# Kernel tuning notes

Measured on AMD Instinct MI355X. Metric: run time of the kernel, lower is better.

The kernel has to match this reference:

```python
import jax, jax.numpy as jnp
import numpy as np

DIM = 384
HEADS = 12
W = 7  # window_size
N = W * W
B = 4096

def _relative_position_index(ws):
    ch = np.arange(ws)
    coords = np.stack(np.meshgrid(ch, ch, indexing='ij'))  # [2, W, W]
    cf = coords.reshape(2, -1)  # [2, W*W]
    rel = cf[:, :, None] - cf[:, None, :]  # [2, N, N]
    rel = rel.transpose(1, 2, 0)
    rel[:, :, 0] += ws - 1
    rel[:, :, 1] += ws - 1
    rel[:, :, 0] *= 2 * ws - 1
    return rel.sum(-1).astype(np.int32)  # [N, N]

def setup_inputs() -> dict:
    key = jax.random.key(0)
    ks = jax.random.split(key, 8)
    s = 0.02
    return {
        'x': jax.random.normal(ks[0], (B, N, DIM), jnp.float32),
        'y': jax.random.normal(ks[1], (B, N, DIM), jnp.float32),
        'q_w': jax.random.normal(ks[2], (DIM, DIM), jnp.float32) * s,
        'q_b': jnp.zeros((DIM,), jnp.float32),
        'kv_w': jax.random.normal(ks[3], (2 * DIM, DIM), jnp.float32) * s,
        'kv_b': jnp.zeros((2 * DIM,), jnp.float32),
        'proj_w': jax.random.normal(ks[4], (DIM, DIM), jnp.float32) * s,
        'proj_b': jnp.zeros((DIM,), jnp.float32),
        'rel_table': jax.random.normal(ks[5], ((2 * W - 1) ** 2, HEADS), jnp.float32) * s,
        'rel_index': jnp.asarray(_relative_position_index(W)),
    }

def reference(x, y, q_w, q_b, kv_w, kv_b, proj_w, proj_b, rel_table, rel_index):
    Bx, N1, C = x.shape
    N2 = y.shape[1]
    hd = C // HEADS
    scale = hd ** -0.5
    # projections (torch Linear: x @ W^T + b)
    q = (x @ q_w.T + q_b).reshape(Bx, N1, HEADS, hd)
    kv = (y @ kv_w.T + kv_b).reshape(Bx, N2, 2, HEADS, hd)
    k = kv[:, :, 0]  # [B, N2, H, d]
    v = kv[:, :, 1]
    attn = jnp.einsum('bqhd,bkhd->bhqk', q, k) * scale
    # relative position bias: [N1, N2, H] -> [H, N1, N2]
    bias = rel_table[rel_index.reshape(-1)].reshape(N1, N2, HEADS)
    attn = attn + jnp.transpose(bias, (2, 0, 1))[None]
    attn = jax.nn.softmax(attn, axis=-1)
    out = jnp.einsum('bhqk,bkhd->bqhd', attn, v).reshape(Bx, N1, C)
    return out @ proj_w.T + proj_b
```

## Files before the change

kernel.cpp:

```cpp
#include <hip/hip_runtime.h>

#define DIM 384
#define HEADS 12
#define HD 32
#define NTOK 49
#define NWIN 4096
#define MTOT (NWIN*NTOK)
#define PSTR 72

typedef __attribute__((ext_vector_type(8))) __bf16 bf16x8;
typedef __attribute__((ext_vector_type(4))) __bf16 bf16x4;
typedef __attribute__((ext_vector_type(4))) float f32x4;

static __device__ __forceinline__ f32x4 mfma16(bf16x8 a, bf16x8 b, f32x4 c) {
  return __builtin_amdgcn_mfma_f32_16x16x32_bf16(a, b, c, 0, 0, 0);
}

static __device__ __forceinline__ void gload_lds16(const void* g, void* l) {
  __builtin_amdgcn_global_load_lds(
      (const __attribute__((address_space(1))) unsigned int*)g,
      (__attribute__((address_space(3))) unsigned int*)l, 16, 0, 0);
}

static __device__ __forceinline__ bf16x4 cvt4(float4 v) {
  bf16x4 t;
  t[0]=(__bf16)v.x; t[1]=(__bf16)v.y; t[2]=(__bf16)v.z; t[3]=(__bf16)v.w;
  return t;
}

__global__ void k_prep(const float* __restrict__ qw, const float* __restrict__ kvw,
                       const float* __restrict__ pw, const float* __restrict__ rel_table,
                       const int* __restrict__ rel_index,
                       __bf16* __restrict__ qw_bf, __bf16* __restrict__ kvw_bf,
                       __bf16* __restrict__ pw_bf, float* __restrict__ bias_pad) {
  int i = blockIdx.x * 256 + threadIdx.x;
  if (i < DIM*DIM)   qw_bf[i] = (__bf16)qw[i];
  if (i < 2*DIM*DIM) kvw_bf[i] = (__bf16)kvw[i];
  if (i < DIM*DIM)   pw_bf[i] = (__bf16)pw[i];
  if (i < HEADS*64*64) {
    int h = i >> 12, rem = i & 4095, q = rem >> 6, k = rem & 63;
    float v;
    if (k >= NTOK)      v = -1e30f;
    else if (q >= NTOK) v = 0.0f;
    else v = rel_table[rel_index[q*NTOK + k] * HEADS + h];
    bias_pad[i] = v;
  }
}

__global__ __launch_bounds__(256, 4) void k_qkv(
    const float* __restrict__ x, const float* __restrict__ y,
    const __bf16* __restrict__ qw_bf, const __bf16* __restrict__ kvw_bf,
    const float* __restrict__ q_b, const float* __restrict__ kv_b,
    __bf16* __restrict__ Qws, __bf16* __restrict__ Kws, __bf16* __restrict__ Vws)
{
  int b = blockIdx.x;
  int orig = (b & 7) * 1764 + (b >> 3);
  int mtile = orig / 9;
  int nt9 = orig - mtile*9;
  const float* A; const __bf16* Bw; const float* bias; __bf16* Cout;
  int wrow0, col0;
  if (nt9 < 3) { A = x; Bw = qw_bf; bias = q_b; Cout = Qws; wrow0 = nt9*128; col0 = wrow0; }
  else {
    A = y; Bw = kvw_bf; bias = kv_b; wrow0 = (nt9-3)*128;
    if (wrow0 < DIM) { Cout = Kws; col0 = wrow0; } else { Cout = Vws; col0 = wrow0 - DIM; }
  }
  bias += wrow0;

  __shared__ __align__(16) __bf16 As[2*128*32];
  __shared__ __align__(16) __bf16 Bs[3*128*32];

  int t = threadIdx.x, lane = t & 63, wave = t >> 6;
  int l15 = lane & 15, g = lane >> 4;
  int wr = (wave >> 1) * 64, wc = (wave & 1) * 64;
  int row0b = mtile*128;

  int c8 = lane & 7;
  int r8 = lane >> 3;
  int swk = (lane >> 4) & 3;
  const float* asrc = A + (size_t)(row0b + wave*32 + r8)*DIM + c8*4;
  unsigned lwb = (unsigned)wave*2048 + (unsigned)r8*64
               + ((((c8 >> 1) ^ swk) << 4) + (c8 & 1)*8);

  int sr  = 2*(lane >> 3) + ((lane >> 2) & 1);
  int scb = (lane & 3) ^ ((lane >> 3) & 3);
  const __bf16* bsrc0 = Bw + (size_t)(wrow0 + (wave*2    )*16 + sr)*DIM + scb*8;
  const __bf16* bsrc1 = Bw + (size_t)(wrow0 + (wave*2 + 1)*16 + sr)*DIM + scb*8;

  f32x4 acc[4][4];
  #pragma unroll
  for (int a=0;a<4;a++)
    #pragma unroll
    for (int bb=0;bb<4;bb++) acc[a][bb] = (f32x4){0.f,0.f,0.f,0.f};

  {
    float4 s0 = *(const float4*)(asrc);
    float4 s1 = *(const float4*)(asrc +  8*DIM);
    float4 s2 = *(const float4*)(asrc + 16*DIM);
    float4 s3 = *(const float4*)(asrc + 24*DIM);
    gload_lds16(bsrc0,      (char*)Bs +        (wave*2  )*1024);
    gload_lds16(bsrc1,      (char*)Bs +        (wave*2+1)*1024);
    gload_lds16(bsrc0 + 32, (char*)Bs + 8192 + (wave*2  )*1024);
    gload_lds16(bsrc1 + 32, (char*)Bs + 8192 + (wave*2+1)*1024);
    *(bf16x4*)((char*)As + lwb +    0) = cvt4(s0);
    *(bf16x4*)((char*)As + lwb +  512) = cvt4(s1);
    *(bf16x4*)((char*)As + lwb + 1024) = cvt4(s2);
    *(bf16x4*)((char*)As + lwb + 1536) = cvt4(s3);
    asm volatile("s_waitcnt vmcnt(2)" ::: "memory");
    asm volatile("s_waitcnt lgkmcnt(0)" ::: "memory");
    __builtin_amdgcn_s_barrier();
  }

  int lslot = l15*64 + ((g ^ ((l15 >> 1) & 3)) << 4);

  #pragma unroll
  for (int kt = 0; kt < 12; ++kt) {
    const int cur2 = kt & 1, nxt2 = cur2 ^ 1;
    const int cur3 = kt % 3, pre3 = (kt + 2) % 3;
    float4 s0, s1, s2, s3;
    if (kt < 11) {
      int kk = (kt + 1) * 32;
      s0 = *(const float4*)(asrc + kk);
      s1 = *(const float4*)(asrc + kk +  8*DIM);
      s2 = *(const float4*)(asrc + kk + 16*DIM);
      s3 = *(const float4*)(asrc + kk + 24*DIM);
    }
    if (kt < 10) {
      int kk = (kt + 2) * 32;
      gload_lds16(bsrc0 + kk, (char*)Bs + pre3*8192 + (wave*2  )*1024);
      gload_lds16(bsrc1 + kk, (char*)Bs + pre3*8192 + (wave*2+1)*1024);
    }
    bf16x8 af[4], bfv[4];
    #pragma unroll
    for (int a=0;a<4;a++)
      af[a]  = *(const bf16x8*)((const char*)As + cur2*8192 + (wr + a*16)*64 + lslot);
    #pragma unroll
    for (int bb=0;bb<4;bb++)
      bfv[bb] = *(const bf16x8*)((const char*)Bs + cur3*8192 + (wc + bb*16)*64 + lslot);
    #pragma unroll
    for (int a=0;a<4;a++)
      #pragma unroll
      for (int bb=0;bb<4;bb++)
        acc[a][bb] = mfma16(af[a], bfv[bb], acc[a][bb]);
    if (kt < 11) {
      *(bf16x4*)((char*)As + nxt2*8192 + lwb +    0) = cvt4(s0);
      *(bf16x4*)((char*)As + nxt2*8192 + lwb +  512) = cvt4(s1);
      *(bf16x4*)((char*)As + nxt2*8192 + lwb + 1024) = cvt4(s2);
      *(bf16x4*)((char*)As + nxt2*8192 + lwb + 1536) = cvt4(s3);
      if (kt < 10) asm volatile("s_waitcnt vmcnt(2)" ::: "memory");
      else         asm volatile("s_waitcnt vmcnt(0)" ::: "memory");
      asm volatile("s_waitcnt lgkmcnt(0)" ::: "memory");
      __builtin_amdgcn_s_barrier();
    }
  }

  #pragma unroll
  for (int a=0;a<4;a++) {
    #pragma unroll
    for (int bb=0;bb<4;bb++) {
      int colw = wc + bb*16 + l15;
      float bi = bias[colw];
      size_t cbase = (size_t)(row0b + wr + a*16 + 4*g)*DIM + (col0 + colw);
      #pragma unroll
      for (int r=0;r<4;r++)
        Cout[cbase + (size_t)r*DIM] = (__bf16)(acc[a][bb][r] + bi);
    }
  }
}

__global__ __launch_bounds__(256) void k_attn(
    __bf16* qao,
    const __bf16* __restrict__ Kws, const __bf16* __restrict__ Vws,
    const float* __restrict__ bias_pad)
{
  __shared__ __align__(16) __bf16 Psh[4][64*PSTR];
  __shared__ __align__(16) __bf16 VTsh[4][32*PSTR];
  int b = blockIdx.x;
  int lane = threadIdx.x & 63, wave = threadIdx.x >> 6;
  int l15 = lane & 15, g = lane >> 4;
  __bf16* Pw  = Psh[wave];
  __bf16* VTw = VTsh[wave];
  size_t rowbase = (size_t)b * NTOK * DIM;
  const float scale = 0.17677669529663687f;

  for (int e = lane; e < 32*15; e += 64) {
    int d = e / 15, k = 49 + (e - d*15);
    VTw[d*PSTR + k] = (__bf16)0.0f;
  }

  for (int hh = 0; hh < 3; hh++) {
    int h = wave + hh*4;
    for (int e = lane; e < NTOK*HD; e += 64) {
      int k = e >> 5, d = e & 31;
      VTw[d*PSTR + k] = Vws[rowbase + (size_t)k*DIM + h*HD + d];
    }
    bf16x8 qf[4], kf[4];
    #pragma unroll
    for (int mt=0; mt<4; mt++) {
      int q = 16*mt + l15; if (q > 48) q = 48;
      qf[mt] = *(const bf16x8*)(qao + rowbase + (size_t)q*DIM + h*HD + g*8);
    }
    #pragma unroll
    for (int nt=0; nt<4; nt++) {
      int kk = 16*nt + l15; if (kk > 48) kk = 48;
      kf[nt] = *(const bf16x8*)(Kws + rowbase + (size_t)kk*DIM + h*HD + g*8);
    }
    f32x4 sacc[4][4];
    #pragma unroll
    for (int mt=0; mt<4; mt++)
      #pragma unroll
      for (int nt=0; nt<4; nt++)
        sacc[mt][nt] = mfma16(qf[mt], kf[nt], (f32x4){0.f,0.f,0.f,0.f});

    const float* bt = bias_pad + h*4096;
    float rs[4][4];
    #pragma unroll
    for (int mt=0; mt<4; mt++) {
      #pragma unroll
      for (int r=0; r<4; r++) {
        int q = 16*mt + 4*g + r;
        float v0 = sacc[mt][0][r]*scale + bt[q*64 +  0 + l15];
        float v1 = sacc[mt][1][r]*scale + bt[q*64 + 16 + l15];
        float v2 = sacc[mt][2][r]*scale + bt[q*64 + 32 + l15];
        float v3 = sacc[mt][3][r]*scale + bt[q*64 + 48 + l15];
        float m = fmaxf(fmaxf(v0,v1), fmaxf(v2,v3));
        #pragma unroll
        for (int off=1; off<16; off<<=1) m = fmaxf(m, __shfl_xor(m, off));
        v0 = __expf(v0-m); v1 = __expf(v1-m); v2 = __expf(v2-m); v3 = __expf(v3-m);
        float s = v0+v1+v2+v3;
        #pragma unroll
        for (int off=1; off<16; off<<=1) s += __shfl_xor(s, off);
        rs[mt][r] = s;
        Pw[q*PSTR +  0 + l15] = (__bf16)v0;
        Pw[q*PSTR + 16 + l15] = (__bf16)v1;
        Pw[q*PSTR + 32 + l15] = (__bf16)v2;
        Pw[q*PSTR + 48 + l15] = (__bf16)v3;
      }
    }

    #pragma unroll
    for (int mt=0; mt<4; mt++) {
      #pragma unroll
      for (int dt=0; dt<2; dt++) {
        f32x4 o = (f32x4){0.f,0.f,0.f,0.f};
        #pragma unroll
        for (int ks=0; ks<2; ks++) {
          bf16x8 pa = *(const bf16x8*)(Pw  + (16*mt + l15)*PSTR + 32*ks + 8*g);
          bf16x8 vb = *(const bf16x8*)(VTw + (16*dt + l15)*PSTR + 32*ks + 8*g);
          o = mfma16(pa, vb, o);
        }
        #pragma unroll
        for (int r=0; r<4; r++) {
          int q = 16*mt + 4*g + r;
          if (q < NTOK)
            qao[rowbase + (size_t)q*DIM + h*HD + 16*dt + l15] = (__bf16)(o[r] / rs[mt][r]);
        }
      }
    }
  }
}

__global__ __launch_bounds__(256, 4) void k_proj(
    const __bf16* __restrict__ Aao, const __bf16* __restrict__ pw_bf,
    const float* __restrict__ pb, float* __restrict__ out)
{
  int b = blockIdx.x;
  int orig = (b & 7) * 588 + (b >> 3);
  int mtile = orig / 3;
  int nt = orig - mtile*3;
  int lane = threadIdx.x & 63, wave = threadIdx.x >> 6;
  int l15 = lane & 15, g = lane >> 4;
  int wr = (wave >> 1) * 64, wc = (wave & 1) * 64;
  int row0b = mtile*128;
  int col00 = nt*128;

  __shared__ __align__(16) __bf16 As[3*128*32];
  __shared__ __align__(16) __bf16 Bs[3*128*32];

  int sr  = 2*(lane >> 3) + ((lane >> 2) & 1);
  int scb = (lane & 3) ^ ((lane >> 3) & 3);
  const __bf16* asrc0 = Aao   + (size_t)(row0b + (wave*2    )*16 + sr)*DIM + scb*8;
  const __bf16* asrc1 = Aao   + (size_t)(row0b + (wave*2 + 1)*16 + sr)*DIM + scb*8;
  const __bf16* bsrc0 = pw_bf + (size_t)(col00 + (wave*2    )*16 + sr)*DIM + scb*8;
  const __bf16* bsrc1 = pw_bf + (size_t)(col00 + (wave*2 + 1)*16 + sr)*DIM + scb*8;

  f32x4 acc[4][4];
  #pragma unroll
  for (int a=0;a<4;a++)
    #pragma unroll
    for (int bb=0;bb<4;bb++) acc[a][bb] = (f32x4){0.f,0.f,0.f,0.f};

  {
    gload_lds16(asrc0,      (char*)As +        (wave*2  )*1024);
    gload_lds16(asrc1,      (char*)As +        (wave*2+1)*1024);
    gload_lds16(bsrc0,      (char*)Bs +        (wave*2  )*1024);
    gload_lds16(bsrc1,      (char*)Bs +        (wave*2+1)*1024);
    gload_lds16(asrc0 + 32, (char*)As + 8192 + (wave*2  )*1024);
    gload_lds16(asrc1 + 32, (char*)As + 8192 + (wave*2+1)*1024);
    gload_lds16(bsrc0 + 32, (char*)Bs + 8192 + (wave*2  )*1024);
    gload_lds16(bsrc1 + 32, (char*)Bs + 8192 + (wave*2+1)*1024);
    asm volatile("s_waitcnt vmcnt(4)" ::: "memory");
    __builtin_amdgcn_s_barrier();
  }

  int lslot = l15*64 + ((g ^ ((l15 >> 1) & 3)) << 4);

  #pragma unroll
  for (int kt = 0; kt < 12; ++kt) {
    const int cur3 = kt % 3, pre3 = (kt + 2) % 3;
    if (kt < 10) {
      int kk = (kt + 2) * 32;
      gload_lds16(asrc0 + kk, (char*)As + pre3*8192 + (wave*2  )*1024);
      gload_lds16(asrc1 + kk, (char*)As + pre3*8192 + (wave*2+1)*1024);
      gload_lds16(bsrc0 + kk, (char*)Bs + pre3*8192 + (wave*2  )*1024);
      gload_lds16(bsrc1 + kk, (char*)Bs + pre3*8192 + (wave*2+1)*1024);
    }
    bf16x8 af[4], bfv[4];
    #pragma unroll
    for (int a=0;a<4;a++)
      af[a]  = *(const bf16x8*)((const char*)As + cur3*8192 + (wr + a*16)*64 + lslot);
    #pragma unroll
    for (int bb=0;bb<4;bb++)
      bfv[bb] = *(const bf16x8*)((const char*)Bs + cur3*8192 + (wc + bb*16)*64 + lslot);
    #pragma unroll
    for (int a=0;a<4;a++)
      #pragma unroll
      for (int bb=0;bb<4;bb++)
        acc[a][bb] = mfma16(af[a], bfv[bb], acc[a][bb]);
    if (kt < 11) {
      if (kt < 10) asm volatile("s_waitcnt vmcnt(4)" ::: "memory");
      else         asm volatile("s_waitcnt vmcnt(0)" ::: "memory");
      __builtin_amdgcn_s_barrier();
    }
  }

  #pragma unroll
  for (int a=0;a<4;a++) {
    #pragma unroll
    for (int bb=0;bb<4;bb++) {
      int col = col00 + wc + bb*16 + l15;
      float bi = pb[col];
      size_t cbase = (size_t)(row0b + wr + a*16 + 4*g)*DIM + col;
      #pragma unroll
      for (int r=0;r<4;r++)
        out[cbase + (size_t)r*DIM] = acc[a][bb][r] + bi;
    }
  }
}

extern "C" void kernel_launch(void* const* d_in, const int* in_sizes, int n_in,
                              void* d_out, int out_size, void* d_ws, size_t ws_size,
                              hipStream_t stream)
{
  const float* x   = (const float*)d_in[0];
  const float* y   = (const float*)d_in[1];
  const float* qw  = (const float*)d_in[2];
  const float* qb  = (const float*)d_in[3];
  const float* kvw = (const float*)d_in[4];
  const float* kvb = (const float*)d_in[5];
  const float* pw  = (const float*)d_in[6];
  const float* pb  = (const float*)d_in[7];
  const float* rt  = (const float*)d_in[8];
  const int*   ri  = (const int*)d_in[9];
  float* out = (float*)d_out;

  char* ws = (char*)d_ws;
  const size_t WS_NEEDED = 1376256ull + 3ull*154140672ull;
  if (ws_size < WS_NEEDED) return;

  __bf16* qw_bf    = (__bf16*)(ws);
  __bf16* kvw_bf   = (__bf16*)(ws + 294912);
  __bf16* pw_bf    = (__bf16*)(ws + 884736);
  float*  bias_pad = (float*)(ws + 1179648);
  __bf16* Qws      = (__bf16*)(ws + 1376256);
  __bf16* Kws      = Qws + (size_t)MTOT*DIM;
  __bf16* Vws      = Kws + (size_t)MTOT*DIM;

  k_prep<<<dim3(1152), dim3(256), 0, stream>>>(qw, kvw, pw, rt, ri, qw_bf, kvw_bf, pw_bf, bias_pad);
  k_qkv <<<dim3(1568*9), dim3(256), 0, stream>>>(x, y, qw_bf, kvw_bf, qb, kvb, Qws, Kws, Vws);
  k_attn<<<dim3(NWIN), dim3(256), 0, stream>>>(Qws, Kws, Vws, bias_pad);
  k_proj<<<dim3(1568*3), dim3(256), 0, stream>>>(Qws, pw_bf, pb, out);
}
```

Before: 840.8 us.

## Store Q/K/V and attention output in head-major per-window layout

The projection GEMM epilogue now writes Q, K and V as [window][head][token][dim], using a magic-number divide by 49 in place of row-major [token][384]. The attention kernel therefore reads each head's data as one contiguous block, with vectorized V loads for the transpose. The output projection reads its A operand from this layout, where each 32-wide K slice is a separate head block. The aim is better coalescing in the attention kernel, at the cost of scattered 2-byte stores in the GEMM epilogue and strided A tile loads in the projection.

```diff
diff --git a/kernel.cpp b/kernel.cpp
--- a/kernel.cpp
+++ b/kernel.cpp
@@ -7,6 +7,8 @@
 #define NWIN 4096
 #define MTOT (NWIN*NTOK)
 #define PSTR 72
+#define WSTR 18816
+#define HSTR 1568
 
 typedef __attribute__((ext_vector_type(8))) __bf16 bf16x8;
 typedef __attribute__((ext_vector_type(4))) __bf16 bf16x4;
@@ -26,6 +28,11 @@
   bf16x4 t;
   t[0]=(__bf16)v.x; t[1]=(__bf16)v.y; t[2]=(__bf16)v.z; t[3]=(__bf16)v.w;
   return t;
+}
+
+static __device__ __forceinline__ void div49(unsigned r, unsigned& w, unsigned& t) {
+  w = (unsigned)(((unsigned long long)r * 1402438302ull) >> 36);
+  t = r - w * 49u;
 }
 
 __global__ void k_prep(const float* __restrict__ qw, const float* __restrict__ kvw,
@@ -153,16 +160,26 @@
     }
   }
 
+  unsigned wo[4][4];
+  #pragma unroll
+  for (int a=0;a<4;a++)
+    #pragma unroll
+    for (int r=0;r<4;r++) {
+      unsigned row = (unsigned)(row0b + wr + a*16 + 4*g + r);
+      unsigned w, tk; div49(row, w, tk);
+      wo[a][r] = w*(unsigned)WSTR + tk*32u;
+    }
   #pragma unroll
   for (int a=0;a<4;a++) {
     #pragma unroll
     for (int bb=0;bb<4;bb++) {
       int colw = wc + bb*16 + l15;
+      int col = col0 + colw;
+      unsigned hb = (unsigned)(col >> 5)*(unsigned)HSTR + (unsigned)(col & 31);
       float bi = bias[colw];
-      size_t cbase = (size_t)(row0b + wr + a*16 + 4*g)*DIM + (col0 + colw);
       #pragma unroll
       for (int r=0;r<4;r++)
-        Cout[cbase + (size_t)r*DIM] = (__bf16)(acc[a][bb][r] + bi);
+        Cout[wo[a][r] + hb] = (__bf16)(acc[a][bb][r] + bi);
     }
   }
 }
@@ -179,7 +196,9 @@
   int l15 = lane & 15, g = lane >> 4;
   __bf16* Pw  = Psh[wave];
   __bf16* VTw = VTsh[wave];
-  size_t rowbase = (size_t)b * NTOK * DIM;
+  __bf16* Qb = qao + (size_t)b * WSTR;
+  const __bf16* Kb = Kws + (size_t)b * WSTR;
+  const __bf16* Vb = Vws + (size_t)b * WSTR;
   const float scale = 0.17677669529663687f;
 
   for (int e = lane; e < 32*15; e += 64) {
@@ -189,20 +208,25 @@
 
   for (int hh = 0; hh < 3; hh++) {
     int h = wave + hh*4;
-    for (int e = lane; e < NTOK*HD; e += 64) {
-      int k = e >> 5, d = e & 31;
-      VTw[d*PSTR + k] = Vws[rowbase + (size_t)k*DIM + h*HD + d];
+    const __bf16* Qh = Qb + h*HSTR;
+    const __bf16* Kh = Kb + h*HSTR;
+    const __bf16* Vh = Vb + h*HSTR;
+    for (int e = lane*8; e < NTOK*HD; e += 512) {
+      bf16x8 v = *(const bf16x8*)(Vh + e);
+      int tok = e >> 5, d0 = e & 31;
+      #pragma unroll
+      for (int i=0;i<8;i++) VTw[(d0+i)*PSTR + tok] = v[i];
     }
     bf16x8 qf[4], kf[4];
     #pragma unroll
     for (int mt=0; mt<4; mt++) {
       int q = 16*mt + l15; if (q > 48) q = 48;
-      qf[mt] = *(const bf16x8*)(qao + rowbase + (size_t)q*DIM + h*HD + g*8);
+      qf[mt] = *(const bf16x8*)(Qh + q*HD + g*8);
     }
     #pragma unroll
     for (int nt=0; nt<4; nt++) {
       int kk = 16*nt + l15; if (kk > 48) kk = 48;
-      kf[nt] = *(const bf16x8*)(Kws + rowbase + (size_t)kk*DIM + h*HD + g*8);
+      kf[nt] = *(const bf16x8*)(Kh + kk*HD + g*8);
     }
     f32x4 sacc[4][4];
     #pragma unroll
@@ -237,6 +261,7 @@
       }
     }
 
+    __bf16* AOh = Qb + h*HSTR;
     #pragma unroll
     for (int mt=0; mt<4; mt++) {
       #pragma unroll
@@ -252,7 +277,7 @@
         for (int r=0; r<4; r++) {
           int q = 16*mt + 4*g + r;
           if (q < NTOK)
-            qao[rowbase + (size_t)q*DIM + h*HD + 16*dt + l15] = (__bf16)(o[r] / rs[mt][r]);
+            AOh[q*HD + 16*dt + l15] = (__bf16)(o[r] / rs[mt][r]);
         }
       }
     }
@@ -278,8 +303,14 @@
 
   int sr  = 2*(lane >> 3) + ((lane >> 2) & 1);
   int scb = (lane & 3) ^ ((lane >> 3) & 3);
-  const __bf16* asrc0 = Aao   + (size_t)(row0b + (wave*2    )*16 + sr)*DIM + scb*8;
-  const __bf16* asrc1 = Aao   + (size_t)(row0b + (wave*2 + 1)*16 + sr)*DIM + scb*8;
+  const __bf16* asrc0; const __bf16* asrc1;
+  {
+    unsigned r0 = (unsigned)(row0b + (wave*2    )*16 + sr);
+    unsigned r1 = (unsigned)(row0b + (wave*2 + 1)*16 + sr);
+    unsigned w0, t0, w1, t1; div49(r0, w0, t0); div49(r1, w1, t1);
+    asrc0 = Aao + (size_t)w0*WSTR + t0*32 + scb*8;
+    asrc1 = Aao + (size_t)w1*WSTR + t1*32 + scb*8;
+  }
   const __bf16* bsrc0 = pw_bf + (size_t)(col00 + (wave*2    )*16 + sr)*DIM + scb*8;
   const __bf16* bsrc1 = pw_bf + (size_t)(col00 + (wave*2 + 1)*16 + sr)*DIM + scb*8;
 
@@ -290,14 +321,14 @@
     for (int bb=0;bb<4;bb++) acc[a][bb] = (f32x4){0.f,0.f,0.f,0.f};
 
   {
-    gload_lds16(asrc0,      (char*)As +        (wave*2  )*1024);
-    gload_lds16(asrc1,      (char*)As +        (wave*2+1)*1024);
-    gload_lds16(bsrc0,      (char*)Bs +        (wave*2  )*1024);
-    gload_lds16(bsrc1,      (char*)Bs +        (wave*2+1)*1024);
-    gload_lds16(asrc0 + 32, (char*)As + 8192 + (wave*2  )*1024);
-    gload_lds16(asrc1 + 32, (char*)As + 8192 + (wave*2+1)*1024);
-    gload_lds16(bsrc0 + 32, (char*)Bs + 8192 + (wave*2  )*1024);
-    gload_lds16(bsrc1 + 32, (char*)Bs + 8192 + (wave*2+1)*1024);
+    gload_lds16(asrc0,        (char*)As +        (wave*2  )*1024);
+    gload_lds16(asrc1,        (char*)As +        (wave*2+1)*1024);
+    gload_lds16(bsrc0,        (char*)Bs +        (wave*2  )*1024);
+    gload_lds16(bsrc1,        (char*)Bs +        (wave*2+1)*1024);
+    gload_lds16(asrc0 + HSTR, (char*)As + 8192 + (wave*2  )*1024);
+    gload_lds16(asrc1 + HSTR, (char*)As + 8192 + (wave*2+1)*1024);
+    gload_lds16(bsrc0 + 32,   (char*)Bs + 8192 + (wave*2  )*1024);
+    gload_lds16(bsrc1 + 32,   (char*)Bs + 8192 + (wave*2+1)*1024);
     asm volatile("s_waitcnt vmcnt(4)" ::: "memory");
     __builtin_amdgcn_s_barrier();
   }
@@ -308,11 +339,12 @@
   for (int kt = 0; kt < 12; ++kt) {
     const int cur3 = kt % 3, pre3 = (kt + 2) % 3;
     if (kt < 10) {
-      int kk = (kt + 2) * 32;
-      gload_lds16(asrc0 + kk, (char*)As + pre3*8192 + (wave*2  )*1024);
-      gload_lds16(asrc1 + kk, (char*)As + pre3*8192 + (wave*2+1)*1024);
-      gload_lds16(bsrc0 + kk, (char*)Bs + pre3*8192 + (wave*2  )*1024);
-      gload_lds16(bsrc1 + kk, (char*)Bs + pre3*8192 + (wave*2+1)*1024);
+      int ka = (kt + 2) * HSTR;
+      int kb = (kt + 2) * 32;
+      gload_lds16(asrc0 + ka, (char*)As + pre3*8192 + (wave*2  )*1024);
+      gload_lds16(asrc1 + ka, (char*)As + pre3*8192 + (wave*2+1)*1024);
+      gload_lds16(bsrc0 + kb, (char*)Bs + pre3*8192 + (wave*2  )*1024);
+      gload_lds16(bsrc1 + kb, (char*)Bs + pre3*8192 + (wave*2+1)*1024);
     }
     bf16x8 af[4], bfv[4];
     #pragma unroll
```

Measured after the change: 1.039 ms. 23.5% more time.

## Enlarge QKV GEMM tile to 256x128 with 512-thread blocks

Applied to the files above, without the earlier changes.

The QKV projection kernel now uses 8 waves per block covering a 256-row M tile instead of 128, with the A tile in LDS doubled and the load mapping and swizzle rewritten so each wave loads rows strided by 64. Each block's B (weight) tile is reused across twice as many rows, and global weight traffic per output is halved. The cost is more LDS per block and more registers under launch bounds of 512 threads with 4 blocks, which may cut occupancy, plus half as many blocks.

```diff
diff --git a/kernel.cpp b/kernel.cpp
--- a/kernel.cpp
+++ b/kernel.cpp
@@ -47,14 +47,14 @@
   }
 }
 
-__global__ __launch_bounds__(256, 4) void k_qkv(
+__global__ __launch_bounds__(512, 4) void k_qkv(
     const float* __restrict__ x, const float* __restrict__ y,
     const __bf16* __restrict__ qw_bf, const __bf16* __restrict__ kvw_bf,
     const float* __restrict__ q_b, const float* __restrict__ kv_b,
     __bf16* __restrict__ Qws, __bf16* __restrict__ Kws, __bf16* __restrict__ Vws)
 {
   int b = blockIdx.x;
-  int orig = (b & 7) * 1764 + (b >> 3);
+  int orig = (b & 7) * 882 + (b >> 3);
   int mtile = orig / 9;
   int nt9 = orig - mtile*9;
   const float* A; const __bf16* Bw; const float* bias; __bf16* Cout;
@@ -66,25 +66,25 @@
   }
   bias += wrow0;
 
-  __shared__ __align__(16) __bf16 As[2*128*32];
+  __shared__ __align__(16) __bf16 As[2*256*32];
   __shared__ __align__(16) __bf16 Bs[3*128*32];
 
   int t = threadIdx.x, lane = t & 63, wave = t >> 6;
   int l15 = lane & 15, g = lane >> 4;
-  int wr = (wave >> 1) * 64, wc = (wave & 1) * 64;
-  int row0b = mtile*128;
+  int wrM = (wave >> 1) * 64;
+  int wcN = (wave & 1) * 64;
+  int row0b = mtile*256;
 
   int c8 = lane & 7;
   int r8 = lane >> 3;
-  int swk = (lane >> 4) & 3;
-  const float* asrc = A + (size_t)(row0b + wave*32 + r8)*DIM + c8*4;
-  unsigned lwb = (unsigned)wave*2048 + (unsigned)r8*64
+  int swk = ((wave*8 + r8) >> 1) & 3;
+  const float* asrc = A + (size_t)(row0b + wave*8 + r8)*DIM + c8*4;
+  unsigned lwb = (unsigned)(wave*8 + r8)*64
                + ((((c8 >> 1) ^ swk) << 4) + (c8 & 1)*8);
 
   int sr  = 2*(lane >> 3) + ((lane >> 2) & 1);
   int scb = (lane & 3) ^ ((lane >> 3) & 3);
-  const __bf16* bsrc0 = Bw + (size_t)(wrow0 + (wave*2    )*16 + sr)*DIM + scb*8;
-  const __bf16* bsrc1 = Bw + (size_t)(wrow0 + (wave*2 + 1)*16 + sr)*DIM + scb*8;
+  const __bf16* bsrc = Bw + (size_t)(wrow0 + wave*16 + sr)*DIM + scb*8;
 
   f32x4 acc[4][4];
   #pragma unroll
@@ -94,18 +94,16 @@
 
   {
     float4 s0 = *(const float4*)(asrc);
-    float4 s1 = *(const float4*)(asrc +  8*DIM);
-    float4 s2 = *(const float4*)(asrc + 16*DIM);
-    float4 s3 = *(const float4*)(asrc + 24*DIM);
-    gload_lds16(bsrc0,      (char*)Bs +        (wave*2  )*1024);
-    gload_lds16(bsrc1,      (char*)Bs +        (wave*2+1)*1024);
-    gload_lds16(bsrc0 + 32, (char*)Bs + 8192 + (wave*2  )*1024);
-    gload_lds16(bsrc1 + 32, (char*)Bs + 8192 + (wave*2+1)*1024);
-    *(bf16x4*)((char*)As + lwb +    0) = cvt4(s0);
-    *(bf16x4*)((char*)As + lwb +  512) = cvt4(s1);
-    *(bf16x4*)((char*)As + lwb + 1024) = cvt4(s2);
-    *(bf16x4*)((char*)As + lwb + 1536) = cvt4(s3);
-    asm volatile("s_waitcnt vmcnt(2)" ::: "memory");
+    float4 s1 = *(const float4*)(asrc +  64*DIM);
+    float4 s2 = *(const float4*)(asrc + 128*DIM);
+    float4 s3 = *(const float4*)(asrc + 192*DIM);
+    gload_lds16(bsrc,      (char*)Bs +        wave*1024);
+    gload_lds16(bsrc + 32, (char*)Bs + 8192 + wave*1024);
+    *(bf16x4*)((char*)As + lwb +     0) = cvt4(s0);
+    *(bf16x4*)((char*)As + lwb +  4096) = cvt4(s1);
+    *(bf16x4*)((char*)As + lwb +  8192) = cvt4(s2);
+    *(bf16x4*)((char*)As + lwb + 12288) = cvt4(s3);
+    asm volatile("s_waitcnt vmcnt(1)" ::: "memory");
     asm volatile("s_waitcnt lgkmcnt(0)" ::: "memory");
     __builtin_amdgcn_s_barrier();
   }
@@ -120,33 +118,32 @@
     if (kt < 11) {
       int kk = (kt + 1) * 32;
       s0 = *(const float4*)(asrc + kk);
-      s1 = *(const float4*)(asrc + kk +  8*DIM);
-      s2 = *(const float4*)(asrc + kk + 16*DIM);
-      s3 = *(const float4*)(asrc + kk + 24*DIM);
-    }
-    if (kt < 10) {
-      int kk = (kt + 2) * 32;
-      gload_lds16(bsrc0 + kk, (char*)Bs + pre3*8192 + (wave*2  )*1024);
-      gload_lds16(bsrc1 + kk, (char*)Bs + pre3*8192 + (wave*2+1)*1024);
-    }
+      s1 = *(const float4*)(asrc + kk +  64*DIM);
+      s2 = *(const float4*)(asrc + kk + 128*DIM);
+      s3 = *(const float4*)(asrc + kk + 192*DIM);
+    }
+    if (kt < 10)
+      gload_lds16(bsrc + (kt + 2)*32, (char*)Bs + pre3*8192 + wave*1024);
+
     bf16x8 af[4], bfv[4];
     #pragma unroll
     for (int a=0;a<4;a++)
-      af[a]  = *(const bf16x8*)((const char*)As + cur2*8192 + (wr + a*16)*64 + lslot);
+      af[a]  = *(const bf16x8*)((const char*)As + cur2*16384 + (wrM + a*16)*64 + lslot);
     #pragma unroll
     for (int bb=0;bb<4;bb++)
-      bfv[bb] = *(const bf16x8*)((const char*)Bs + cur3*8192 + (wc + bb*16)*64 + lslot);
+      bfv[bb] = *(const bf16x8*)((const char*)Bs + cur3*8192 + (wcN + bb*16)*64 + lslot);
     #pragma unroll
     for (int a=0;a<4;a++)
       #pragma unroll
       for (int bb=0;bb<4;bb++)
         acc[a][bb] = mfma16(af[a], bfv[bb], acc[a][bb]);
+
     if (kt < 11) {
-      *(bf16x4*)((char*)As + nxt2*8192 + lwb +    0) = cvt4(s0);
-      *(bf16x4*)((char*)As + nxt2*8192 + lwb +  512) = cvt4(s1);
-      *(bf16x4*)((char*)As + nxt2*8192 + lwb + 1024) = cvt4(s2);
-      *(bf16x4*)((char*)As + nxt2*8192 + lwb + 1536) = cvt4(s3);
-      if (kt < 10) asm volatile("s_waitcnt vmcnt(2)" ::: "memory");
+      *(bf16x4*)((char*)As + nxt2*16384 + lwb +     0) = cvt4(s0);
+      *(bf16x4*)((char*)As + nxt2*16384 + lwb +  4096) = cvt4(s1);
+      *(bf16x4*)((char*)As + nxt2*16384 + lwb +  8192) = cvt4(s2);
+      *(bf16x4*)((char*)As + nxt2*16384 + lwb + 12288) = cvt4(s3);
+      if (kt < 10) asm volatile("s_waitcnt vmcnt(1)" ::: "memory");
       else         asm volatile("s_waitcnt vmcnt(0)" ::: "memory");
       asm volatile("s_waitcnt lgkmcnt(0)" ::: "memory");
       __builtin_amdgcn_s_barrier();
@@ -157,9 +154,9 @@
   for (int a=0;a<4;a++) {
     #pragma unroll
     for (int bb=0;bb<4;bb++) {
-      int colw = wc + bb*16 + l15;
+      int colw = wcN + bb*16 + l15;
       float bi = bias[colw];
-      size_t cbase = (size_t)(row0b + wr + a*16 + 4*g)*DIM + (col0 + colw);
+      size_t cbase = (size_t)(row0b + wrM + a*16 + 4*g)*DIM + (col0 + colw);
       #pragma unroll
       for (int r=0;r<4;r++)
         Cout[cbase + (size_t)r*DIM] = (__bf16)(acc[a][bb][r] + bi);
@@ -376,7 +373,7 @@
   __bf16* Vws      = Kws + (size_t)MTOT*DIM;
 
   k_prep<<<dim3(1152), dim3(256), 0, stream>>>(qw, kvw, pw, rt, ri, qw_bf, kvw_bf, pw_bf, bias_pad);
-  k_qkv <<<dim3(1568*9), dim3(256), 0, stream>>>(x, y, qw_bf, kvw_bf, qb, kvb, Qws, Kws, Vws);
+  k_qkv <<<dim3(784*9), dim3(512), 0, stream>>>(x, y, qw_bf, kvw_bf, qb, kvb, Qws, Kws, Vws);
   k_attn<<<dim3(NWIN), dim3(256), 0, stream>>>(Qws, Kws, Vws, bias_pad);
   k_proj<<<dim3(1568*3), dim3(256), 0, stream>>>(Qws, pw_bf, pb, out);
 }
```

Measured after the change: 851.6 us. Within noise of the previous version (+1.3%).

## Fuse attention and output projection into one per-window kernel

Applied to the files above, without the earlier changes.

Merges the attention kernel and the separate output-projection GEMM. Each window's attention output now stays in an LDS buffer (64 rows, padded stride) instead of being written to global memory and read back. After a block barrier, each wave computes 96 output columns for the window and streams proj weights straight from global/L2 with register double-buffering. The P scratch is cut to a 16-row tile per m-tile so the larger LDS footprint fits two blocks per CU. The risks are lower occupancy, proj weights re-read from cache by every window, and a less efficient 49-row GEMM tile compared with the tuned 128x128 LDS-pipelined GEMM.

```diff
diff --git a/kernel.cpp b/kernel.cpp
--- a/kernel.cpp
+++ b/kernel.cpp
@@ -7,6 +7,7 @@
 #define NWIN 4096
 #define MTOT (NWIN*NTOK)
 #define PSTR 72
+#define ASTR 392
 
 typedef __attribute__((ext_vector_type(8))) __bf16 bf16x8;
 typedef __attribute__((ext_vector_type(4))) __bf16 bf16x4;
@@ -167,13 +168,15 @@
   }
 }
 
-__global__ __launch_bounds__(256) void k_attn(
-    __bf16* qao,
-    const __bf16* __restrict__ Kws, const __bf16* __restrict__ Vws,
-    const float* __restrict__ bias_pad)
+__global__ __launch_bounds__(256, 2) void k_attnproj(
+    const __bf16* __restrict__ Qws, const __bf16* __restrict__ Kws,
+    const __bf16* __restrict__ Vws, const float* __restrict__ bias_pad,
+    const __bf16* __restrict__ pw_bf, const float* __restrict__ pb,
+    float* __restrict__ out)
 {
-  __shared__ __align__(16) __bf16 Psh[4][64*PSTR];
   __shared__ __align__(16) __bf16 VTsh[4][32*PSTR];
+  __shared__ __align__(16) __bf16 Psh[4][16*PSTR];
+  __shared__ __align__(16) __bf16 AOB[64*ASTR];
   int b = blockIdx.x;
   int lane = threadIdx.x & 63, wave = threadIdx.x >> 6;
   int l15 = lane & 15, g = lane >> 4;
@@ -197,7 +200,7 @@
     #pragma unroll
     for (int mt=0; mt<4; mt++) {
       int q = 16*mt + l15; if (q > 48) q = 48;
-      qf[mt] = *(const bf16x8*)(qao + rowbase + (size_t)q*DIM + h*HD + g*8);
+      qf[mt] = *(const bf16x8*)(Qws + rowbase + (size_t)q*DIM + h*HD + g*8);
     }
     #pragma unroll
     for (int nt=0; nt<4; nt++) {
@@ -212,12 +215,13 @@
         sacc[mt][nt] = mfma16(qf[mt], kf[nt], (f32x4){0.f,0.f,0.f,0.f});
 
     const float* bt = bias_pad + h*4096;
-    float rs[4][4];
     #pragma unroll
     for (int mt=0; mt<4; mt++) {
+      float rs[4];
       #pragma unroll
       for (int r=0; r<4; r++) {
         int q = 16*mt + 4*g + r;
+        int qloc = 4*g + r;
         float v0 = sacc[mt][0][r]*scale + bt[q*64 +  0 + l15];
         float v1 = sacc[mt][1][r]*scale + bt[q*64 + 16 + l15];
         float v2 = sacc[mt][2][r]*scale + bt[q*64 + 32 + l15];
@@ -229,120 +233,76 @@
         float s = v0+v1+v2+v3;
         #pragma unroll
         for (int off=1; off<16; off<<=1) s += __shfl_xor(s, off);
-        rs[mt][r] = s;
-        Pw[q*PSTR +  0 + l15] = (__bf16)v0;
-        Pw[q*PSTR + 16 + l15] = (__bf16)v1;
-        Pw[q*PSTR + 32 + l15] = (__bf16)v2;
-        Pw[q*PSTR + 48 + l15] = (__bf16)v3;
+        rs[r] = s;
+        Pw[qloc*PSTR +  0 + l15] = (__bf16)v0;
+        Pw[qloc*PSTR + 16 + l15] = (__bf16)v1;
+        Pw[qloc*PSTR + 32 + l15] = (__bf16)v2;
+        Pw[qloc*PSTR + 48 + l15] = (__bf16)v3;
       }
-    }
-
-    #pragma unroll
-    for (int mt=0; mt<4; mt++) {
       #pragma unroll
       for (int dt=0; dt<2; dt++) {
         f32x4 o = (f32x4){0.f,0.f,0.f,0.f};
         #pragma unroll
         for (int ks=0; ks<2; ks++) {
-          bf16x8 pa = *(const bf16x8*)(Pw  + (16*mt + l15)*PSTR + 32*ks + 8*g);
+          bf16x8 pa = *(const bf16x8*)(Pw  + l15*PSTR + 32*ks + 8*g);
           bf16x8 vb = *(const bf16x8*)(VTw + (16*dt + l15)*PSTR + 32*ks + 8*g);
           o = mfma16(pa, vb, o);
         }
         #pragma unroll
         for (int r=0; r<4; r++) {
-          int q = 16*mt + 4*g + r;
-          if (q < NTOK)
-            qao[rowbase + (size_t)q*DIM + h*HD + 16*dt + l15] = (__bf16)(o[r] / rs[mt][r]);
+          int tok = 16*mt + 4*g + r;
+          AOB[(unsigned)tok*ASTR + h*HD + 16*dt + l15] = (__bf16)(o[r] / rs[r]);
         }
       }
     }
   }
-}
-
-__global__ __launch_bounds__(256, 4) void k_proj(
-    const __bf16* __restrict__ Aao, const __bf16* __restrict__ pw_bf,
-    const float* __restrict__ pb, float* __restrict__ out)
-{
-  int b = blockIdx.x;
-  int orig = (b & 7) * 588 + (b >> 3);
-  int mtile = orig / 3;
-  int nt = orig - mtile*3;
-  int lane = threadIdx.x & 63, wave = threadIdx.x >> 6;
-  int l15 = lane & 15, g = lane >> 4;
-  int wr = (wave >> 1) * 64, wc = (wave & 1) * 64;
-  int row0b = mtile*128;
-  int col00 = nt*128;
-
-  __shared__ __align__(16) __bf16 As[3*128*32];
-  __shared__ __align__(16) __bf16 Bs[3*128*32];
-
-  int sr  = 2*(lane >> 3) + ((lane >> 2) & 1);
-  int scb = (lane & 3) ^ ((lane >> 3) & 3);
-  const __bf16* asrc0 = Aao   + (size_t)(row0b + (wave*2    )*16 + sr)*DIM + scb*8;
-  const __bf16* asrc1 = Aao   + (size_t)(row0b + (wave*2 + 1)*16 + sr)*DIM + scb*8;
-  const __bf16* bsrc0 = pw_bf + (size_t)(col00 + (wave*2    )*16 + sr)*DIM + scb*8;
-  const __bf16* bsrc1 = pw_bf + (size_t)(col00 + (wave*2 + 1)*16 + sr)*DIM + scb*8;
-
-  f32x4 acc[4][4];
-  #pragma unroll
-  for (int a=0;a<4;a++)
-    #pragma unroll
-    for (int bb=0;bb<4;bb++) acc[a][bb] = (f32x4){0.f,0.f,0.f,0.f};
+  __syncthreads();
 
   {
-    gload_lds16(asrc0,      (char*)As +        (wave*2  )*1024);
-    gload_lds16(asrc1,      (char*)As +        (wave*2+1)*1024);
-    gload_lds16(bsrc0,      (char*)Bs +        (wave*2  )*1024);
-    gload_lds16(bsrc1,      (char*)Bs +        (wave*2+1)*1024);
-    gload_lds16(asrc0 + 32, (char*)As + 8192 + (wave*2  )*1024);
-    gload_lds16(asrc1 + 32, (char*)As + 8192 + (wave*2+1)*1024);
-    gload_lds16(bsrc0 + 32, (char*)Bs + 8192 + (wave*2  )*1024);
-    gload_lds16(bsrc1 + 32, (char*)Bs + 8192 + (wave*2+1)*1024);
-    asm volatile("s_waitcnt vmcnt(4)" ::: "memory");
-    __builtin_amdgcn_s_barrier();
-  }
-
-  int lslot = l15*64 + ((g ^ ((l15 >> 1) & 3)) << 4);
-
-  #pragma unroll
-  for (int kt = 0; kt < 12; ++kt) {
-    const int cur3 = kt % 3, pre3 = (kt + 2) % 3;
-    if (kt < 10) {
-      int kk = (kt + 2) * 32;
-      gload_lds16(asrc0 + kk, (char*)As + pre3*8192 + (wave*2  )*1024);
-      gload_lds16(asrc1 + kk, (char*)As + pre3*8192 + (wave*2+1)*1024);
-      gload_lds16(bsrc0 + kk, (char*)Bs + pre3*8192 + (wave*2  )*1024);
-      gload_lds16(bsrc1 + kk, (char*)Bs + pre3*8192 + (wave*2+1)*1024);
-    }
-    bf16x8 af[4], bfv[4];
+    f32x4 acc[4][6];
     #pragma unroll
     for (int a=0;a<4;a++)
-      af[a]  = *(const bf16x8*)((const char*)As + cur3*8192 + (wr + a*16)*64 + lslot);
-    #pragma unroll
-    for (int bb=0;bb<4;bb++)
-      bfv[bb] = *(const bf16x8*)((const char*)Bs + cur3*8192 + (wc + bb*16)*64 + lslot);
-    #pragma unroll
-    for (int a=0;a<4;a++)
-      #pragma unroll
-      for (int bb=0;bb<4;bb++)
-        acc[a][bb] = mfma16(af[a], bfv[bb], acc[a][bb]);
-    if (kt < 11) {
-      if (kt < 10) asm volatile("s_waitcnt vmcnt(4)" ::: "memory");
-      else         asm volatile("s_waitcnt vmcnt(0)" ::: "memory");
-      __builtin_amdgcn_s_barrier();
-    }
-  }
-
-  #pragma unroll
-  for (int a=0;a<4;a++) {
-    #pragma unroll
-    for (int bb=0;bb<4;bb++) {
-      int col = col00 + wc + bb*16 + l15;
-      float bi = pb[col];
-      size_t cbase = (size_t)(row0b + wr + a*16 + 4*g)*DIM + col;
-      #pragma unroll
-      for (int r=0;r<4;r++)
-        out[cbase + (size_t)r*DIM] = acc[a][bb][r] + bi;
+      #pragma unroll
+      for (int j=0;j<6;j++) acc[a][j] = (f32x4){0.f,0.f,0.f,0.f};
+    const __bf16* bptr[6];
+    #pragma unroll
+    for (int j=0;j<6;j++)
+      bptr[j] = pw_bf + (size_t)(96*wave + 16*j + l15)*DIM + g*8;
+    bf16x8 bc[6];
+    #pragma unroll
+    for (int j=0;j<6;j++) bc[j] = *(const bf16x8*)(bptr[j]);
+
+    #pragma unroll
+    for (int kt = 0; kt < 12; ++kt) {
+      bf16x8 bn[6];
+      if (kt < 11) {
+        #pragma unroll
+        for (int j=0;j<6;j++) bn[j] = *(const bf16x8*)(bptr[j] + (kt+1)*32);
+      }
+      bf16x8 af[4];
+      #pragma unroll
+      for (int a=0;a<4;a++)
+        af[a] = *(const bf16x8*)(AOB + (unsigned)(16*a + l15)*ASTR + kt*32 + g*8);
+      #pragma unroll
+      for (int a=0;a<4;a++)
+        #pragma unroll
+        for (int j=0;j<6;j++)
+          acc[a][j] = mfma16(af[a], bc[j], acc[a][j]);
+      #pragma unroll
+      for (int j=0;j<6;j++) bc[j] = bn[j];
+    }
+    #pragma unroll
+    for (int j=0;j<6;j++) {
+      const int col = 96*wave + 16*j + l15;
+      const float bi = pb[col];
+      #pragma unroll
+      for (int a=0;a<4;a++)
+        #pragma unroll
+        for (int r=0;r<4;r++) {
+          const int tok = 16*a + 4*g + r;
+          if (tok < NTOK)
+            out[((size_t)b*NTOK + tok)*DIM + col] = acc[a][j][r] + bi;
+        }
     }
   }
 }
@@ -375,8 +335,7 @@
   __bf16* Kws      = Qws + (size_t)MTOT*DIM;
   __bf16* Vws      = Kws + (size_t)MTOT*DIM;
 
-  k_prep<<<dim3(1152), dim3(256), 0, stream>>>(qw, kvw, pw, rt, ri, qw_bf, kvw_bf, pw_bf, bias_pad);
-  k_qkv <<<dim3(1568*9), dim3(256), 0, stream>>>(x, y, qw_bf, kvw_bf, qb, kvb, Qws, Kws, Vws);
-  k_attn<<<dim3(NWIN), dim3(256), 0, stream>>>(Qws, Kws, Vws, bias_pad);
-  k_proj<<<dim3(1568*3), dim3(256), 0, stream>>>(Qws, pw_bf, pb, out);
-}
+  k_prep    <<<dim3(1152), dim3(256), 0, stream>>>(qw, kvw, pw, rt, ri, qw_bf, kvw_bf, pw_bf, bias_pad);
+  k_qkv     <<<dim3(1568*9), dim3(256), 0, stream>>>(x, y, qw_bf, kvw_bf, qb, kvb, Qws, Kws, Vws);
+  k_attnproj<<<dim3(NWIN), dim3(256), 0, stream>>>(Qws, Kws, Vws, bias_pad, pw_bf, pb, out);
+}
```

Result: no change. 851.1 us (+1.2%).
